# Performance work log

Hardware: AMD Instinct MI355X
Metric: run time of the kernel (lower is better)

## Reference

```python
import jax, jax.numpy as jnp
import numpy as np

IN_FEATURES = 4096
OUT_FEATURES = 14336
TOKENS = 32


def setup_inputs() -> dict:
    key = jax.random.key(0)
    k1, k2, k3 = jax.random.split(key, 3)
    x = jax.random.normal(k1, (TOKENS, IN_FEATURES), dtype=jnp.float32)
    # int8-valued quantized weight stored as int32 (symmetric Q8, range [-127, 127])
    weight = jax.random.randint(k2, (OUT_FEATURES, IN_FEATURES), -127, 128, dtype=jnp.int32)
    # per-in-feature (per-column of [out,in] matrix) positive scales
    scales = jax.random.uniform(k3, (IN_FEATURES,), dtype=jnp.float32, minval=0.001, maxval=0.02)
    return {"x": x, "weight": weight, "scales": scales}


def reference(x, weight, scales):
    # Original torch: dequant[o,i] = weight[o,i] * scales[i]; out = x @ dequant.T
    # Equivalent fused form: out[t,o] = sum_i (x[t,i]*scales[i]) * weight[o,i]
    x_scaled = x * scales[None, :]            # [T, in]
    w = weight.astype(jnp.float32)            # [out, in]
    out = jnp.einsum('ti,oi->to', x_scaled, w)  # [T, out]
    return out
```

## Files before the change

### kernel.cpp

```cpp
#include <hip/hip_runtime.h>
#include <stdint.h>
#include <stddef.h>

#define IN_F   4096
#define OUT_F  14336
#define TOK    32

#define OTILE  64
#define ISPLIT 16
#define IBLK   (IN_F / ISPLIT)
#define KBPB   (IBLK / 32)

typedef __attribute__((ext_vector_type(8))) short bf16x8;
typedef __attribute__((ext_vector_type(4))) float f32x4;

__global__ __launch_bounds__(256) void prep_kernel(
    const float* __restrict__ x, const float* __restrict__ scales,
    int4* __restrict__ xfrag, float* __restrict__ out)
{
    const int f = blockIdx.x * 256 + threadIdx.x;
    if (f < (TOK * IN_F / 8)) {
        const int t  = f >> 9;
        const int i8 = f & 511;
        const int kb = i8 >> 2;
        const int kg = i8 & 3;
        const float4* xp = (const float4*)(x + (size_t)t * IN_F + i8 * 8);
        const float4* sp = (const float4*)(scales + i8 * 8);
        float4 x0 = xp[0], x1 = xp[1];
        float4 s0 = sp[0], s1 = sp[1];
        float v[8] = { x0.x*s0.x, x0.y*s0.y, x0.z*s0.z, x0.w*s0.w,
                       x1.x*s1.x, x1.y*s1.y, x1.z*s1.z, x1.w*s1.w };
        uint32_t h[8];
#pragma unroll
        for (int j = 0; j < 8; ++j) {
            uint32_t b = __float_as_uint(v[j]);
            b += 0x7fffu + ((b >> 16) & 1u);
            h[j] = b >> 16;
        }
        int4 d;
        d.x = (int)(h[0] | (h[1] << 16));
        d.y = (int)(h[2] | (h[3] << 16));
        d.z = (int)(h[4] | (h[5] << 16));
        d.w = (int)(h[6] | (h[7] << 16));
        xfrag[((kb * 2 + (t >> 4)) * 64) + kg * 16 + (t & 15)] = d;
    }
    if (f < (OUT_F * TOK / 4)) {
        ((float4*)out)[f] = make_float4(0.f, 0.f, 0.f, 0.f);
    }
}

__global__ __launch_bounds__(256, 4) void qgemm_kernel(
    const int* __restrict__ wgt, const int4* __restrict__ xfrag,
    float* __restrict__ out)
{
    const int lane = threadIdx.x & 63;
    const int wv   = threadIdx.x >> 6;
    const int lx   = lane & 15;
    const int quad = lane >> 4;
    const int ob   = blockIdx.x * OTILE + wv * 16;
    const int ib0  = blockIdx.y * IBLK;

    int4 a[KBPB][2];
#pragma unroll
    for (int kb = 0; kb < KBPB; ++kb)
#pragma unroll
        for (int mt = 0; mt < 2; ++mt)
            a[kb][mt] = xfrag[((blockIdx.y * KBPB + kb) * 2 + mt) * 64 + lane];

    f32x4 acc[2] = { {0.f,0.f,0.f,0.f}, {0.f,0.f,0.f,0.f} };

    const int* wp = wgt + (size_t)(ob + lx) * IN_F + ib0 + quad * 8;

#pragma unroll
    for (int kb = 0; kb < KBPB; ++kb) {
        const int4 w0 = *(const int4*)(wp + kb * 32);
        const int4 w1 = *(const int4*)(wp + kb * 32 + 4);
        bf16x8 b;
        b[0] = (short)(__float_as_uint((float)w0.x) >> 16);
        b[1] = (short)(__float_as_uint((float)w0.y) >> 16);
        b[2] = (short)(__float_as_uint((float)w0.z) >> 16);
        b[3] = (short)(__float_as_uint((float)w0.w) >> 16);
        b[4] = (short)(__float_as_uint((float)w1.x) >> 16);
        b[5] = (short)(__float_as_uint((float)w1.y) >> 16);
        b[6] = (short)(__float_as_uint((float)w1.z) >> 16);
        b[7] = (short)(__float_as_uint((float)w1.w) >> 16);
        bf16x8 a0, a1;
        __builtin_memcpy(&a0, &a[kb][0], 16);
        __builtin_memcpy(&a1, &a[kb][1], 16);
        acc[0] = __builtin_amdgcn_mfma_f32_16x16x32_bf16(a0, b, acc[0], 0, 0, 0);
        acc[1] = __builtin_amdgcn_mfma_f32_16x16x32_bf16(a1, b, acc[1], 0, 0, 0);
    }

#pragma unroll
    for (int mt = 0; mt < 2; ++mt)
#pragma unroll
        for (int reg = 0; reg < 4; ++reg) {
            const int t = mt * 16 + quad * 4 + reg;
            atomicAdd(&out[(size_t)t * OUT_F + ob + lx], acc[mt][reg]);
        }
}

extern "C" void kernel_launch(void* const* d_in, const int* in_sizes, int n_in,
                              void* d_out, int out_size, void* d_ws, size_t ws_size,
                              hipStream_t stream)
{
    const float* x      = (const float*)d_in[0];
    const int*   wgt    = (const int*)d_in[1];
    const float* scales = (const float*)d_in[2];
    float* out = (float*)d_out;
    int4*  xfrag = (int4*)d_ws;

    prep_kernel<<<dim3((TOK * IN_F) / 256), 256, 0, stream>>>(x, scales, xfrag, out);

    dim3 grid(OUT_F / OTILE, ISPLIT);
    qgemm_kernel<<<grid, 256, 0, stream>>>(wgt, xfrag, out);
}
```

Before: 331.6 us.

## Replace split-K atomics with in-block 4-wave K reduction via shared memory

Each block now owns a 16-column output tile, and its four waves each cover one quarter of K. Partial sums are reduced through shared memory and written with plain stores. This removes the global atomicAdd traffic and the output zeroing in the prep kernel, and the prep grid shrinks to the threads it actually needs. In exchange, activation fragments are loaded inside the K loop instead of preloaded into registers, and the grid becomes 896 blocks with long serial K loops per wave.

```diff
diff --git a/kernel.cpp b/kernel.cpp
--- a/kernel.cpp
+++ b/kernel.cpp
@@ -6,73 +6,63 @@
 #define OUT_F  14336
 #define TOK    32
 
-#define OTILE  64
-#define ISPLIT 16
-#define IBLK   (IN_F / ISPLIT)
-#define KBPB   (IBLK / 32)
+#define OTILE  16
+#define KWAVE  (IN_F / 4)
+#define KBW    (KWAVE / 32)
 
 typedef __attribute__((ext_vector_type(8))) short bf16x8;
 typedef __attribute__((ext_vector_type(4))) float f32x4;
 
 __global__ __launch_bounds__(256) void prep_kernel(
     const float* __restrict__ x, const float* __restrict__ scales,
-    int4* __restrict__ xfrag, float* __restrict__ out)
+    int4* __restrict__ xfrag)
 {
     const int f = blockIdx.x * 256 + threadIdx.x;
-    if (f < (TOK * IN_F / 8)) {
-        const int t  = f >> 9;
-        const int i8 = f & 511;
-        const int kb = i8 >> 2;
-        const int kg = i8 & 3;
-        const float4* xp = (const float4*)(x + (size_t)t * IN_F + i8 * 8);
-        const float4* sp = (const float4*)(scales + i8 * 8);
-        float4 x0 = xp[0], x1 = xp[1];
-        float4 s0 = sp[0], s1 = sp[1];
-        float v[8] = { x0.x*s0.x, x0.y*s0.y, x0.z*s0.z, x0.w*s0.w,
-                       x1.x*s1.x, x1.y*s1.y, x1.z*s1.z, x1.w*s1.w };
-        uint32_t h[8];
+    const int t  = f >> 9;
+    const int i8 = f & 511;
+    const int kb = i8 >> 2;
+    const int kg = i8 & 3;
+    const float4* xp = (const float4*)(x + (size_t)t * IN_F + i8 * 8);
+    const float4* sp = (const float4*)(scales + i8 * 8);
+    float4 x0 = xp[0], x1 = xp[1];
+    float4 s0 = sp[0], s1 = sp[1];
+    float v[8] = { x0.x*s0.x, x0.y*s0.y, x0.z*s0.z, x0.w*s0.w,
+                   x1.x*s1.x, x1.y*s1.y, x1.z*s1.z, x1.w*s1.w };
+    uint32_t h[8];
 #pragma unroll
-        for (int j = 0; j < 8; ++j) {
-            uint32_t b = __float_as_uint(v[j]);
-            b += 0x7fffu + ((b >> 16) & 1u);
-            h[j] = b >> 16;
-        }
-        int4 d;
-        d.x = (int)(h[0] | (h[1] << 16));
-        d.y = (int)(h[2] | (h[3] << 16));
-        d.z = (int)(h[4] | (h[5] << 16));
-        d.w = (int)(h[6] | (h[7] << 16));
-        xfrag[((kb * 2 + (t >> 4)) * 64) + kg * 16 + (t & 15)] = d;
+    for (int j = 0; j < 8; ++j) {
+        uint32_t b = __float_as_uint(v[j]);
+        b += 0x7fffu + ((b >> 16) & 1u);
+        h[j] = b >> 16;
     }
-    if (f < (OUT_F * TOK / 4)) {
-        ((float4*)out)[f] = make_float4(0.f, 0.f, 0.f, 0.f);
-    }
+    int4 d;
+    d.x = (int)(h[0] | (h[1] << 16));
+    d.y = (int)(h[2] | (h[3] << 16));
+    d.z = (int)(h[4] | (h[5] << 16));
+    d.w = (int)(h[6] | (h[7] << 16));
+    xfrag[((kb * 2 + (t >> 4)) * 64) + kg * 16 + (t & 15)] = d;
 }
 
 __global__ __launch_bounds__(256, 4) void qgemm_kernel(
     const int* __restrict__ wgt, const int4* __restrict__ xfrag,
     float* __restrict__ out)
 {
+    __shared__ float lred[4][8][64];
     const int lane = threadIdx.x & 63;
     const int wv   = threadIdx.x >> 6;
     const int lx   = lane & 15;
     const int quad = lane >> 4;
-    const int ob   = blockIdx.x * OTILE + wv * 16;
-    const int ib0  = blockIdx.y * IBLK;
+    const int o0   = blockIdx.x * OTILE;
 
-    int4 a[KBPB][2];
-#pragma unroll
-    for (int kb = 0; kb < KBPB; ++kb)
-#pragma unroll
-        for (int mt = 0; mt < 2; ++mt)
-            a[kb][mt] = xfrag[((blockIdx.y * KBPB + kb) * 2 + mt) * 64 + lane];
+    const int* wp = wgt + (size_t)(o0 + lx) * IN_F + wv * KWAVE + quad * 8;
+    const int4* ap = xfrag + ((size_t)wv * KBW) * 2 * 64 + lane;
 
     f32x4 acc[2] = { {0.f,0.f,0.f,0.f}, {0.f,0.f,0.f,0.f} };
 
-    const int* wp = wgt + (size_t)(ob + lx) * IN_F + ib0 + quad * 8;
-
-#pragma unroll
-    for (int kb = 0; kb < KBPB; ++kb) {
+#pragma unroll 8
+    for (int kb = 0; kb < KBW; ++kb) {
+        int4 av0 = ap[(kb * 2 + 0) * 64];
+        int4 av1 = ap[(kb * 2 + 1) * 64];
         const int4 w0 = *(const int4*)(wp + kb * 32);
         const int4 w1 = *(const int4*)(wp + kb * 32 + 4);
         bf16x8 b;
@@ -85,19 +75,26 @@
         b[6] = (short)(__float_as_uint((float)w1.z) >> 16);
         b[7] = (short)(__float_as_uint((float)w1.w) >> 16);
         bf16x8 a0, a1;
-        __builtin_memcpy(&a0, &a[kb][0], 16);
-        __builtin_memcpy(&a1, &a[kb][1], 16);
+        __builtin_memcpy(&a0, &av0, 16);
+        __builtin_memcpy(&a1, &av1, 16);
         acc[0] = __builtin_amdgcn_mfma_f32_16x16x32_bf16(a0, b, acc[0], 0, 0, 0);
         acc[1] = __builtin_amdgcn_mfma_f32_16x16x32_bf16(a1, b, acc[1], 0, 0, 0);
     }
 
 #pragma unroll
-    for (int mt = 0; mt < 2; ++mt)
+    for (int s = 0; s < 8; ++s)
+        lred[wv][s][lane] = acc[s >> 2][s & 3];
+    __syncthreads();
+
+    if (wv == 0) {
 #pragma unroll
-        for (int reg = 0; reg < 4; ++reg) {
-            const int t = mt * 16 + quad * 4 + reg;
-            atomicAdd(&out[(size_t)t * OUT_F + ob + lx], acc[mt][reg]);
+        for (int s = 0; s < 8; ++s) {
+            const float v = lred[0][s][lane] + lred[1][s][lane]
+                          + lred[2][s][lane] + lred[3][s][lane];
+            const int t = (s >> 2) * 16 + quad * 4 + (s & 3);
+            out[(size_t)t * OUT_F + o0 + lx] = v;
         }
+    }
 }
 
 extern "C" void kernel_launch(void* const* d_in, const int* in_sizes, int n_in,
@@ -110,8 +107,7 @@
     float* out = (float*)d_out;
     int4*  xfrag = (int4*)d_ws;
 
-    prep_kernel<<<dim3((TOK * IN_F) / 256), 256, 0, stream>>>(x, scales, xfrag, out);
+    prep_kernel<<<dim3((TOK * IN_F / 8) / 256), 256, 0, stream>>>(x, scales, xfrag);
 
-    dim3 grid(OUT_F / OTILE, ISPLIT);
-    qgemm_kernel<<<grid, 256, 0, stream>>>(wgt, xfrag, out);
+    qgemm_kernel<<<dim3(OUT_F / OTILE), 256, 0, stream>>>(wgt, xfrag, out);
 }
```

New measurement: 336.0 us. About the same (+1.3%).
